# Kernel tuning notes

Measured on AMD Instinct MI355X. Metric: run time of the kernel, lower is better.

Reference implementation:

```python
import jax, jax.numpy as jnp
import numpy as np

EPS_COS = 1e-8   # torch F.cosine_similarity eps
EPS_LN = 1e-6    # LayerNorm eps from source


def _attn_block(x, spat, roi, W, b, k):
    """MultiHeadedAttention_3 (flag=1) forward.
    x: [B,N,C], spat: [B,N,2], roi: [B,N,N], W: [h, 2C+4], b: [h].
    query[b,i,j]=x[b,j], key[b,i,j]=x[b,i]; ft = cat(query,key,spat_q,spat_k).
    The linear over the concat is split into per-part einsums (same math,
    avoids materializing the [B,N,N,2C+4] tensor).
    Returns attn1 * roi * topk-scatter mask, shape [B,N,N,h] (dims b,i,j,h).
    """
    B, N, C = x.shape
    Wq, Wk = W[:, :C], W[:, C:2 * C]
    Wsq, Wsk = W[:, 2 * C:2 * C + 2], W[:, 2 * C + 2:]
    qt = jnp.einsum('bjc,hc->bjh', x, Wq) + jnp.einsum('bjs,hs->bjh', spat, Wsq)
    kt = jnp.einsum('bic,hc->bih', x, Wk) + jnp.einsum('bis,hs->bih', spat, Wsk)
    logits = qt[:, None, :, :] + kt[:, :, None, :] + b  # [B,i,j,h]
    attn1 = jax.nn.sigmoid(logits)
    # relu(cosine_similarity(query, key, dim=3)) -> [B,i,j] (symmetric)
    xn = x / jnp.maximum(jnp.linalg.norm(x, axis=-1, keepdims=True), EPS_COS)
    scores = jax.nn.relu(jnp.einsum('bic,bjc->bij', xn, xn))
    # torch: atten_mask[:, :, idces, :] = 1.0 with idces [B,N,k,1] sets, for ALL
    # b,i,h, column j to 1 whenever j appears anywhere in idces (global scatter).
    _, idx = jax.lax.top_k(scores, k)  # [B,N,k]
    present = jnp.zeros((N,), x.dtype).at[idx.reshape(-1)].set(1.0)
    return attn1 * roi[:, :, :, None] * present[None, None, :, None]


def _gconv_relu(x, w, bias):
    """Grouped 1x1 Conv1d + ReLU. x: [B,Cin,N], w: [g, Cout/g, Cin/g]."""
    B, Cin, N = x.shape
    g, og, ig = w.shape
    y = jnp.einsum('bgin,goi->bgon', x.reshape(B, g, ig, N), w)
    return jax.nn.relu(y.reshape(B, g * og, N) + bias[None, :, None])


def _forward(input, masks_roi, score_mask, spat, W1, b1, W2, b2,
             cw1, cb1, cw2, cb2, ln_g, ln_b, node_num):
    B, N, C = input.shape
    h = W1.shape[0]
    masks = masks_roi * score_mask[:, None, :]
    f = (score_mask == 0).astype(input.dtype)          # [B,N]
    f_mask = f[:, :, None] * jnp.eye(N, dtype=input.dtype)  # diag_embed

    A1 = (_attn_block(input, spat, masks, W1, b1, node_num)
          + f_mask[:, :, :, None]) / 4.0               # [B,i,j,h]

    out1 = _gconv_relu(jnp.swapaxes(input, 1, 2), cw1, cb1)  # [B,mid,N]
    mid = out1.shape[1]
    # torch: matmul(out1.view(B,h,mid/h,N), A1.permute(0,3,2,1))  ([B,h,j,i])
    out1m = jnp.einsum('bhdj,bijh->bhdi', out1.reshape(B, h, mid // h, N), A1)
    out1 = out1 + out1m.reshape(B, mid, N)

    x2 = jnp.swapaxes(out1, 1, 2)                      # [B,N,mid]
    A2 = (_attn_block(x2, spat, masks, W2, b2, node_num)
          + f_mask[:, :, :, None]) / 4.0

    out2 = _gconv_relu(out1, cw2, cb2)                 # [B,out,N]
    co = out2.shape[1]
    out2m = jnp.einsum('bhdj,bijh->bhdi', out2.reshape(B, h, co // h, N), A2)
    out2m = jnp.swapaxes(out2m.reshape(B, co, N), 1, 2)  # [B,N,out]
    mu = jnp.mean(out2m, axis=-1, keepdims=True)
    var = jnp.mean(jnp.square(out2m - mu), axis=-1, keepdims=True)
    out2m = (out2m - mu) / jnp.sqrt(var + EPS_LN) * ln_g + ln_b
    out2 = out2 + jnp.swapaxes(out2m, 1, 2)
    return jnp.swapaxes(out2, 1, 2)                    # [B,N,out]


def setup_inputs() -> dict:
    key = jax.random.key(0)
    ks = jax.random.split(key, 10)
    B, N, C, MID, OUT, H, G = 8, 1024, 256, 256, 256, 4, 4
    s = 0.05
    return {
        'input': jax.random.normal(ks[0], (B, N, C), jnp.float32),
        'masks_roi': jax.random.randint(ks[1], (B, N, N), 0, 2).astype(jnp.float32),
        'score_mask': jax.random.randint(ks[2], (B, N), 0, 2).astype(jnp.float32),
        'spat': jax.random.uniform(ks[3], (B, N, 2), jnp.float32),
        'W1': s * jax.random.normal(ks[4], (H, 2 * C + 4), jnp.float32),
        'b1': jnp.zeros((H,), jnp.float32),
        'W2': s * jax.random.normal(ks[5], (H, 2 * MID + 4), jnp.float32),
        'b2': jnp.zeros((H,), jnp.float32),
        'cw1': s * jax.random.normal(ks[6], (G, MID // G, C // G), jnp.float32),
        'cb1': jnp.zeros((MID,), jnp.float32),
        'cw2': s * jax.random.normal(ks[7], (G, OUT // G, MID // G), jnp.float32),
        'cb2': jnp.zeros((OUT,), jnp.float32),
        'ln_g': jnp.ones((OUT,), jnp.float32),
        'ln_b': jnp.zeros((OUT,), jnp.float32),
        'node_num': 16,
    }


def reference(input, masks_roi, score_mask, spat, W1, b1, W2, b2,
              cw1, cb1, cw2, cb2, ln_g, ln_b, node_num):
    return _forward(input, masks_roi, score_mask, spat, W1, b1, W2, b2,
                    cw1, cb1, cw2, cb2, ln_g, ln_b, node_num)
```

## Files before the change

### kernel.cpp

```cpp
#include <hip/hip_runtime.h>

constexpr int Bb = 8;
constexpr int Nn = 1024;
constexpr int Cc = 256;
constexpr int Hh = 4;
constexpr int WROW = 2 * Cc + 4;

typedef float fx4 __attribute__((ext_vector_type(4)));
typedef float f32x4 __attribute__((ext_vector_type(4)));
typedef __bf16 bf16x8 __attribute__((ext_vector_type(8)));

#define GLL16(src, dst)                                                      \
  __builtin_amdgcn_global_load_lds(                                          \
      (const __attribute__((address_space(1))) void*)(src),                  \
      (__attribute__((address_space(3))) void*)(dst), 16, 0, 0)

__global__ __launch_bounds__(256) void k_roipack(const float* __restrict__ roi,
                                                 const float* __restrict__ sm,
                                                 unsigned long long* __restrict__ roib) {
  __shared__ short jmapS[1024];
  __shared__ int cntS;
  const int t = threadIdx.x;
  const int gid = blockIdx.x * 4 + (t >> 6);
  const int b = gid >> 10;
  const int l = t & 63;
  if ((t >> 6) == 0) {
    int base = 0;
#pragma unroll
    for (int jc = 0; jc < 16; ++jc) {
      const int j = jc * 64 + l;
      const bool act = sm[b * Nn + j] != 0.f;
      const unsigned long long m = __ballot(act);
      if (act) jmapS[base + __popcll(m & ((1ull << l) - 1))] = (short)j;
      base += __popcll(m);
    }
    if (l == 0) cntS = base;
  }
  __syncthreads();
  const int cnt = cntS;
  const float* rrow = roi + (size_t)gid * Nn;
  unsigned long long* orow = roib + (size_t)gid * 16;
#pragma unroll 4
  for (int pc = 0; pc < 16; ++pc) {
    const int idx = pc * 64 + l;
    const bool valid = idx < cnt;
    const int j = valid ? jmapS[idx] : 0;
    const bool bit = valid && (rrow[j] != 0.f);
    unsigned long long m = __ballot(bit);
    if (l == 0) orow[pc] = m;
  }
}

template <int STAGE>
__global__ __launch_bounds__(256) void k_gconvq(const float* __restrict__ src,
                                                const float* __restrict__ cw,
                                                const float* __restrict__ cb,
                                                const float* __restrict__ sm,
                                                const float* __restrict__ spat,
                                                const float* __restrict__ W,
                                                const float* __restrict__ bias,
                                                float* __restrict__ out,
                                                __bf16* __restrict__ gsm,
                                                float* __restrict__ qt,
                                                float* __restrict__ kt) {
  __shared__ __align__(16) bf16x8 xsB[32][32];
  __shared__ float cbS[256];
  __shared__ float smS[32];
  __shared__ int pcolS[32];
  __shared__ int actS[32];
  const int b = blockIdx.x, tile = blockIdx.y;
  const int n0 = tile * 32;
  const int t = threadIdx.x, w = t >> 6, l = t & 63;

  if (w == 0) {
    const int fullc = n0 >> 6;
    int cbase = 0;
    unsigned long long am = 0;
    for (int jc = 0; jc <= fullc; ++jc) {
      unsigned long long m = __ballot(sm[b * Nn + jc * 64 + l] != 0.f);
      if (jc < fullc) cbase += __popcll(m); else am = m;
    }
    const int lsel = l - (n0 & 63);
    if (lsel >= 0 && lsel < 32) {
      pcolS[lsel] = cbase + __popcll(am & ((1ull << l) - 1));
      actS[lsel] = (int)((am >> l) & 1);
      smS[lsel] = 0.25f * sm[b * Nn + n0 + lsel];
    }
  }
  cbS[t] = cb[t];

  if (STAGE == 0) {
    const int n = t >> 3, c0 = (t & 7) * 32;
    const float* srow = src + ((size_t)(b * Nn + n0 + n)) * Cc + c0;
#pragma unroll
    for (int k = 0; k < 4; ++k) {
      fx4 v0 = *(const fx4*)&srow[k * 8];
      fx4 v1 = *(const fx4*)&srow[k * 8 + 4];
      bf16x8 bv;
#pragma unroll
      for (int e = 0; e < 4; ++e) { bv[e] = (__bf16)v0[e]; bv[4 + e] = (__bf16)v1[e]; }
      xsB[n][((c0 >> 3) + k) ^ (n & 7)] = bv;
    }
  } else {
#pragma unroll
    for (int rr = 0; rr < 8; ++rr) {
      const int c = rr * 32 + (t >> 3);
      const int nq = (t & 7) * 4;
      fx4 v = *(const fx4*)&src[((size_t)(b * Cc + c)) * Nn + n0 + nq];
#pragma unroll
      for (int j = 0; j < 4; ++j) {
        const int n = nq + j;
        __bf16* row = (__bf16*)&xsB[n][(c >> 3) ^ (n & 7)];
        row[c & 7] = (__bf16)v[j];
      }
    }
  }
  __syncthreads();

  const int g = w, dl = l & 15, q = l >> 4;

  bf16x8 a[4][2];
#pragma unroll
  for (int of = 0; of < 4; ++of)
#pragma unroll
    for (int ks = 0; ks < 2; ++ks) {
      const float* cwp = cw + ((size_t)(g * 64 + of * 16 + dl)) * 64 + ks * 32 + q * 8;
      fx4 c0 = *(const fx4*)cwp;
      fx4 c1 = *(const fx4*)(cwp + 4);
#pragma unroll
      for (int e = 0; e < 4; ++e) { a[of][ks][e] = (__bf16)c0[e]; a[of][ks][4 + e] = (__bf16)c1[e]; }
    }
  f32x4 acc[4][2] = {};
#pragma unroll
  for (int nf = 0; nf < 2; ++nf) {
    const int n = nf * 16 + dl;
#pragma unroll
    for (int ks = 0; ks < 2; ++ks) {
      bf16x8 bv = xsB[n][(g * 8 + ks * 4 + q) ^ (n & 7)];
#pragma unroll
      for (int of = 0; of < 4; ++of)
        acc[of][nf] = __builtin_amdgcn_mfma_f32_16x16x32_bf16(a[of][ks], bv, acc[of][nf], 0, 0, 0);
    }
  }
#pragma unroll
  for (int of = 0; of < 4; ++of)
#pragma unroll
    for (int nf = 0; nf < 2; ++nf) {
      const int n = nf * 16 + dl;
      const float smv = smS[n];
      const int act = actS[n];
      const int pc = pcolS[n];
#pragma unroll
      for (int r = 0; r < 4; ++r) {
        const int co = g * 64 + of * 16 + 4 * q + r;
        const float val = fmaxf(acc[of][nf][r] + cbS[co], 0.f);
        const size_t orow = ((size_t)(b * Cc + co)) * Nn;
        out[orow + n0 + n] = val;
        if (act) gsm[orow + pc] = (__bf16)(smv * val);
      }
    }

  {
    const int nl = l & 31, half = l >> 5;
    const float* wq = W + g * WROW;
    const float* wk = wq + Cc;
    float qa = 0.f, ka = 0.f;
#pragma unroll 8
    for (int c2 = 0; c2 < 64; ++c2) {
      const int c = half * 128 + c2 * 2;
      const __bf16* p = (const __bf16*)&xsB[nl][(c >> 3) ^ (nl & 7)] + (c & 7);
      const float x0 = (float)p[0], x1 = (float)p[1];
      qa = fmaf(x0, wq[c], fmaf(x1, wq[c + 1], qa));
      ka = fmaf(x0, wk[c], fmaf(x1, wk[c + 1], ka));
    }
    qa += __shfl_xor(qa, 32, 64);
    ka += __shfl_xor(ka, 32, 64);
    if (l < 32) {
      const int n = n0 + nl;
      const float s0 = spat[(b * Nn + n) * 2 + 0];
      const float s1 = spat[(b * Nn + n) * 2 + 1];
      const float* wsp = W + g * WROW + 2 * Cc;
      const float qf = qa + s0 * wsp[0] + s1 * wsp[1] + bias[g];
      const float kf = ka + s0 * wsp[2] + s1 * wsp[3];
      kt[(b * Hh + g) * Nn + n] = kf * -1.44269504f;
      if (actS[nl]) qt[(b * Hh + g) * Nn + pcolS[nl]] = qf * -1.44269504f;
    }
  }
}

template <int MODE>
__global__ __launch_bounds__(512, 4) void k_apply7(const float* __restrict__ g,
                                                   const __bf16* __restrict__ gsm,
                                                   const float* __restrict__ qt,
                                                   const float* __restrict__ kt,
                                                   const unsigned char* __restrict__ roib,
                                                   const float* __restrict__ sm,
                                                   float* __restrict__ out) {
  __shared__ __align__(16) __bf16 Bs[2][3][2][2048];
  __shared__ __align__(16) float qts[1024];
  __shared__ __align__(16) unsigned char rbs[64 * 128];
  const int b = blockIdx.x, it = blockIdx.y, h = blockIdx.z;
  const int t = threadIdx.x, w = t >> 6, l = t & 63;
  const int grp = w >> 2, wq = w & 3;
  const int i0 = it * 64;
  const int dl = l & 15, q = l >> 4, jqf = q * 8;
  const int iA = i0 + wq * 16 + dl;

  const float kvn = kt[(b * Hh + h) * Nn + iA];
  const float* smrow = sm + b * Nn;

  int cnt = 0;
#pragma unroll
  for (int jc = 0; jc < 16; ++jc)
    cnt += __popcll(__ballot(smrow[jc * 64 + l] != 0.f));
  const int stepsTot = (cnt + 63) >> 6;
  const int S = (stepsTot + 1) >> 1;
  const int c0 = grp * S;

  const __bf16* gsrc = gsm + ((size_t)(b * Cc + h * 64 + wq * 16 + (l >> 2))) * Nn
                       + c0 * 64 + (l & 3) * 8;
  __bf16* ring = &Bs[grp][0][0][0];
  const int wdst = wq * 512;

  {
    const float2 qv = *(const float2*)&qt[(b * Hh + h) * Nn + t * 2];
    qts[t * 2 + 0] = qv.x;
    qts[t * 2 + 1] = qv.y;
  }
  {
    const int r = t >> 3, c = (t & 7) * 16;
    const char* src = (const char*)roib + ((size_t)(b * Nn + i0 + r)) * 128 + c;
    *(int4*)&rbs[r * 128 + c] = *(const int4*)src;
  }
  GLL16(gsrc, ring + 0 * 4096 + 0 * 2048 + wdst);
  GLL16(gsrc + 32, ring + 0 * 4096 + 1 * 2048 + wdst);
  GLL16(gsrc + 64, ring + 1 * 4096 + 0 * 2048 + wdst);
  GLL16(gsrc + 96, ring + 1 * 4096 + 1 * 2048 + wdst);
  __syncthreads();

  const int rbbase = (wq * 16 + dl) * 128;
  f32x4 acc[4] = {};
  int cur = 0;

  for (int s = 0; s < S; ++s) {
    const int ck = c0 + s;
    const unsigned int rb0 = rbs[rbbase + ck * 8 + q];
    const unsigned int rb1 = rbs[rbbase + ck * 8 + 4 + q];
    bf16x8 af0, af1;
    {
      fx4 qa = *(const fx4*)&qts[ck * 64 + jqf];
      fx4 qb = *(const fx4*)&qts[ck * 64 + jqf + 4];
#pragma unroll
      for (int e = 0; e < 4; ++e) {
        float sg = __builtin_amdgcn_rcpf(1.f + __builtin_amdgcn_exp2f(qa[e] + kvn));
        af0[e] = (__bf16)(((rb0 >> e) & 1) ? sg : 0.f);
      }
#pragma unroll
      for (int e = 0; e < 4; ++e) {
        float sg = __builtin_amdgcn_rcpf(1.f + __builtin_amdgcn_exp2f(qb[e] + kvn));
        af0[4 + e] = (__bf16)(((rb0 >> (4 + e)) & 1) ? sg : 0.f);
      }
      fx4 qc = *(const fx4*)&qts[ck * 64 + 32 + jqf];
      fx4 qd = *(const fx4*)&qts[ck * 64 + 32 + jqf + 4];
#pragma unroll
      for (int e = 0; e < 4; ++e) {
        float sg = __builtin_amdgcn_rcpf(1.f + __builtin_amdgcn_exp2f(qc[e] + kvn));
        af1[e] = (__bf16)(((rb1 >> e) & 1) ? sg : 0.f);
      }
#pragma unroll
      for (int e = 0; e < 4; ++e) {
        float sg = __builtin_amdgcn_rcpf(1.f + __builtin_amdgcn_exp2f(qd[e] + kvn));
        af1[4 + e] = (__bf16)(((rb1 >> (4 + e)) & 1) ? sg : 0.f);
      }
    }
    asm volatile("s_waitcnt vmcnt(2)\n\ts_barrier" ::: "memory");
    __builtin_amdgcn_sched_barrier(0);
    {
      const int nc = s + 2;
      const int off = (nc < S) ? nc * 64 : 0;
      const int pf = (cur == 0) ? 2 : cur - 1;
      GLL16(gsrc + off, ring + pf * 4096 + 0 * 2048 + wdst);
      GLL16(gsrc + off + 32, ring + pf * 4096 + 1 * 2048 + wdst);
    }
    const __bf16* bp = ring + cur * 4096;
#pragma unroll
    for (int nf = 0; nf < 4; ++nf) {
      bf16x8 bv = *(const bf16x8*)(bp + (nf * 16 + dl) * 32 + jqf);
      acc[nf] = __builtin_amdgcn_mfma_f32_16x16x32_bf16(af0, bv, acc[nf], 0, 0, 0);
    }
#pragma unroll
    for (int nf = 0; nf < 4; ++nf) {
      bf16x8 bv = *(const bf16x8*)(bp + 2048 + (nf * 16 + dl) * 32 + jqf);
      acc[nf] = __builtin_amdgcn_mfma_f32_16x16x32_bf16(af1, bv, acc[nf], 0, 0, 0);
    }
    cur = (cur == 2) ? 0 : cur + 1;
  }

  __syncthreads();
  float* accS = (float*)&Bs[0][0][0][0];
  if (grp == 1) {
#pragma unroll
    for (int nf = 0; nf < 4; ++nf)
      *(f32x4*)&accS[((wq * 64 + l) * 4 + nf) * 4] = acc[nf];
  }
  __syncthreads();
  if (grp == 0) {
#pragma unroll
    for (int nf = 0; nf < 4; ++nf)
      acc[nf] += *(const f32x4*)&accS[((wq * 64 + l) * 4 + nf) * 4];

    const int iw = i0 + wq * 16 + (l >> 4) * 4;
    fx4 sv = *(const fx4*)&smrow[iw];
    float fv[4];
#pragma unroll
    for (int r = 0; r < 4; ++r) fv[r] = (sv[r] == 0.f) ? 0.25f : 0.f;
    if (MODE == 0) {
#pragma unroll
      for (int nf = 0; nf < 4; ++nf) {
        const int ch = h * 64 + nf * 16 + dl;
        const size_t base = ((size_t)(b * Cc + ch)) * Nn + iw;
        fx4 gv = *(const fx4*)&g[base];
        fx4 res;
#pragma unroll
        for (int r = 0; r < 4; ++r) res[r] = gv[r] * (1.f + fv[r]) + acc[nf][r];
        *(fx4*)&out[base] = res;
      }
    } else {
#pragma unroll
      for (int nf = 0; nf < 4; ++nf) {
        const int ch = h * 64 + nf * 16 + dl;
        fx4 gv = *(const fx4*)&g[((size_t)(b * Cc + ch)) * Nn + iw];
#pragma unroll
        for (int r = 0; r < 4; ++r)
          out[((size_t)b * Nn + iw + r) * Cc + ch] = acc[nf][r] + fv[r] * gv[r];
      }
    }
  }
}

__global__ __launch_bounds__(256) void k_lnfinal(float* __restrict__ io,
                                                 const float* __restrict__ g2,
                                                 const float* __restrict__ lng,
                                                 const float* __restrict__ lnb) {
  __shared__ float gt[32][258];
  const int b = blockIdx.x, i0 = blockIdx.y * 32;
  const int t = threadIdx.x, w = t >> 6, l = t & 63;
  {
    const int n = t & 31, ch = t >> 5;
#pragma unroll 8
    for (int rr = 0; rr < 32; ++rr) {
      int c = rr * 8 + ch;
      gt[n][c] = g2[((size_t)(b * Cc + c)) * Nn + i0 + n];
    }
  }
  __syncthreads();
  const fx4 lngv = *(const fx4*)&lng[l * 4];
  const fx4 lnbv = *(const fx4*)&lnb[l * 4];
#pragma unroll
  for (int r = 0; r < 8; ++r) {
    const int n = r * 4 + w;
    const size_t base = ((size_t)(b * Nn) + i0 + n) * Cc + l * 4;
    fx4 v = *(const fx4*)&io[base];
    float s = v[0] + v[1] + v[2] + v[3];
    float sq = v[0] * v[0] + v[1] * v[1] + v[2] * v[2] + v[3] * v[3];
#pragma unroll
    for (int off = 32; off; off >>= 1) {
      s += __shfl_xor(s, off, 64);
      sq += __shfl_xor(sq, off, 64);
    }
    const float m = s * (1.f / 256.f);
    const float var = sq * (1.f / 256.f) - m * m;
    const float rstd = rsqrtf(fmaxf(var, 0.f) + 1e-6f);
    fx4 gv = *(const fx4*)&gt[n][l * 4];
    fx4 res;
#pragma unroll
    for (int e = 0; e < 4; ++e)
      res[e] = gv[e] + (v[e] - m) * rstd * lngv[e] + lnbv[e];
    *(fx4*)&io[base] = res;
  }
}

extern "C" void kernel_launch(void* const* d_in, const int* in_sizes, int n_in,
                              void* d_out, int out_size, void* d_ws, size_t ws_size,
                              hipStream_t stream) {
  (void)in_sizes; (void)n_in; (void)out_size; (void)ws_size;
  const float* input = (const float*)d_in[0];
  const float* roi   = (const float*)d_in[1];
  const float* sm    = (const float*)d_in[2];
  const float* spat  = (const float*)d_in[3];
  const float* W1    = (const float*)d_in[4];
  const float* b1    = (const float*)d_in[5];
  const float* W2    = (const float*)d_in[6];
  const float* b2    = (const float*)d_in[7];
  const float* cw1   = (const float*)d_in[8];
  const float* cb1   = (const float*)d_in[9];
  const float* cw2   = (const float*)d_in[10];
  const float* cb2   = (const float*)d_in[11];
  const float* lng   = (const float*)d_in[12];
  const float* lnb   = (const float*)d_in[13];

  float* outf = (float*)d_out;
  char* ws = (char*)d_ws;
  const size_t PLANE = (size_t)Bb * Cc * Nn;
  float* gbuf = (float*)ws;
  __bf16* gsm = (__bf16*)(ws + PLANE * 4);
  unsigned long long* roib =
      (unsigned long long*)(ws + PLANE * 4 + PLANE * 2);
  float* qtb = (float*)((char*)roib + (size_t)Bb * Nn * 128);
  float* ktb = qtb + Bb * Hh * Nn;
  float* out1 = outf;

  k_roipack<<<dim3(2048), 256, 0, stream>>>(roi, sm, roib);
  k_gconvq<0><<<dim3(8, 32), 256, 0, stream>>>(input, cw1, cb1, sm, spat, W1, b1,
                                               gbuf, gsm, qtb, ktb);
  k_apply7<0><<<dim3(8, 16, 4), 512, 0, stream>>>(gbuf, gsm, qtb, ktb,
                                                  (const unsigned char*)roib, sm, out1);
  k_gconvq<1><<<dim3(8, 32), 256, 0, stream>>>(out1, cw2, cb2, sm, spat, W2, b2,
                                               gbuf, gsm, qtb, ktb);
  k_apply7<1><<<dim3(8, 16, 4), 512, 0, stream>>>(gbuf, gsm, qtb, ktb,
                                                  (const unsigned char*)roib, sm, outf);
  k_lnfinal<<<dim3(8, 32), 256, 0, stream>>>(outf, gbuf, lng, lnb);
}
```

Baseline: 76.59 us.

## Fuse roi bit-packing into first grouped-conv kernel and precompute active counts

Merges the roi-packing kernel into the stage-0 grouped conv/qk kernel as extra blocks (2304 blocks total), removing one launch and letting both workloads share the device. The roi row is now read coalesced into ballot bitmasks in shared memory before compaction, replacing the previous gather reads. The per-batch active count is stored once and read by the apply kernels instead of being recomputed with 16 ballots. STAGE templating is split into two explicit kernels. The roipack blocks are heavy relative to the conv blocks, which may cause imbalance.

Result: slower. 85.57 us (+11.7%).

```diff
diff --git a/kernel.cpp b/kernel.cpp
--- a/kernel.cpp
+++ b/kernel.cpp
@@ -15,62 +15,74 @@
       (const __attribute__((address_space(1))) void*)(src),                  \
       (__attribute__((address_space(3))) void*)(dst), 16, 0, 0)
 
-__global__ __launch_bounds__(256) void k_roipack(const float* __restrict__ roi,
-                                                 const float* __restrict__ sm,
-                                                 unsigned long long* __restrict__ roib) {
-  __shared__ short jmapS[1024];
-  __shared__ int cntS;
-  const int t = threadIdx.x;
-  const int gid = blockIdx.x * 4 + (t >> 6);
-  const int b = gid >> 10;
-  const int l = t & 63;
-  if ((t >> 6) == 0) {
-    int base = 0;
-#pragma unroll
-    for (int jc = 0; jc < 16; ++jc) {
-      const int j = jc * 64 + l;
-      const bool act = sm[b * Nn + j] != 0.f;
-      const unsigned long long m = __ballot(act);
-      if (act) jmapS[base + __popcll(m & ((1ull << l) - 1))] = (short)j;
-      base += __popcll(m);
-    }
-    if (l == 0) cntS = base;
-  }
-  __syncthreads();
-  const int cnt = cntS;
-  const float* rrow = roi + (size_t)gid * Nn;
-  unsigned long long* orow = roib + (size_t)gid * 16;
-#pragma unroll 4
-  for (int pc = 0; pc < 16; ++pc) {
-    const int idx = pc * 64 + l;
-    const bool valid = idx < cnt;
-    const int j = valid ? jmapS[idx] : 0;
-    const bool bit = valid && (rrow[j] != 0.f);
-    unsigned long long m = __ballot(bit);
-    if (l == 0) orow[pc] = m;
-  }
-}
-
-template <int STAGE>
-__global__ __launch_bounds__(256) void k_gconvq(const float* __restrict__ src,
-                                                const float* __restrict__ cw,
-                                                const float* __restrict__ cb,
-                                                const float* __restrict__ sm,
-                                                const float* __restrict__ spat,
-                                                const float* __restrict__ W,
-                                                const float* __restrict__ bias,
-                                                float* __restrict__ out,
-                                                __bf16* __restrict__ gsm,
-                                                float* __restrict__ qt,
-                                                float* __restrict__ kt) {
+__global__ __launch_bounds__(256) void k_gcq0(const float* __restrict__ src,
+                                              const float* __restrict__ cw,
+                                              const float* __restrict__ cb,
+                                              const float* __restrict__ sm,
+                                              const float* __restrict__ spat,
+                                              const float* __restrict__ W,
+                                              const float* __restrict__ bias,
+                                              float* __restrict__ out,
+                                              __bf16* __restrict__ gsm,
+                                              float* __restrict__ qt,
+                                              float* __restrict__ kt,
+                                              const float* __restrict__ roi,
+                                              unsigned long long* __restrict__ roib,
+                                              int* __restrict__ cntb) {
   __shared__ __align__(16) bf16x8 xsB[32][32];
   __shared__ float cbS[256];
   __shared__ float smS[32];
   __shared__ int pcolS[32];
   __shared__ int actS[32];
-  const int b = blockIdx.x, tile = blockIdx.y;
+  __shared__ short jmapS[1024];
+  __shared__ unsigned long long mwS[4][16];
+  __shared__ int cntS;
+
+  const int t = threadIdx.x, w = t >> 6, l = t & 63;
+
+  if (blockIdx.x >= 256) {
+    const int vb2 = blockIdx.x - 256;
+    const int gid = vb2 * 4 + w;
+    const int b = gid >> 10;
+    if (w == 0) {
+      int base = 0;
+#pragma unroll
+      for (int jc = 0; jc < 16; ++jc) {
+        const int j = jc * 64 + l;
+        const bool act = sm[b * Nn + j] != 0.f;
+        const unsigned long long m = __ballot(act);
+        if (act) jmapS[base + __popcll(m & ((1ull << l) - 1))] = (short)j;
+        base += __popcll(m);
+      }
+      if (l == 0) {
+        cntS = base;
+        if ((vb2 & 255) == 0) cntb[b] = base;
+      }
+    }
+    const float* rrow = roi + (size_t)gid * Nn;
+#pragma unroll 4
+    for (int jc = 0; jc < 16; ++jc) {
+      unsigned long long m = __ballot(rrow[jc * 64 + l] != 0.f);
+      if (l == 0) mwS[w][jc] = m;
+    }
+    __syncthreads();
+    const int cnt = cntS;
+    unsigned long long* orow = roib + (size_t)gid * 16;
+#pragma unroll 4
+    for (int pc = 0; pc < 16; ++pc) {
+      const int idx = pc * 64 + l;
+      const bool valid = idx < cnt;
+      const int j = valid ? (int)jmapS[idx] : 0;
+      const bool bit = valid && ((mwS[w][j >> 6] >> (j & 63)) & 1);
+      unsigned long long m = __ballot(bit);
+      if (l == 0) orow[pc] = m;
+    }
+    return;
+  }
+
+  const int vb = blockIdx.x;
+  const int b = vb & 7, tile = vb >> 3;
   const int n0 = tile * 32;
-  const int t = threadIdx.x, w = t >> 6, l = t & 63;
 
   if (w == 0) {
     const int fullc = n0 >> 6;
@@ -89,7 +101,7 @@
   }
   cbS[t] = cb[t];
 
-  if (STAGE == 0) {
+  {
     const int n = t >> 3, c0 = (t & 7) * 32;
     const float* srow = src + ((size_t)(b * Nn + n0 + n)) * Cc + c0;
 #pragma unroll
@@ -100,19 +112,6 @@
 #pragma unroll
       for (int e = 0; e < 4; ++e) { bv[e] = (__bf16)v0[e]; bv[4 + e] = (__bf16)v1[e]; }
       xsB[n][((c0 >> 3) + k) ^ (n & 7)] = bv;
-    }
-  } else {
-#pragma unroll
-    for (int rr = 0; rr < 8; ++rr) {
-      const int c = rr * 32 + (t >> 3);
-      const int nq = (t & 7) * 4;
-      fx4 v = *(const fx4*)&src[((size_t)(b * Cc + c)) * Nn + n0 + nq];
-#pragma unroll
-      for (int j = 0; j < 4; ++j) {
-        const int n = nq + j;
-        __bf16* row = (__bf16*)&xsB[n][(c >> 3) ^ (n & 7)];
-        row[c & 7] = (__bf16)v[j];
-      }
     }
   }
   __syncthreads();
@@ -188,6 +187,127 @@
   }
 }
 
+__global__ __launch_bounds__(256) void k_gconvq1(const float* __restrict__ src,
+                                                 const float* __restrict__ cw,
+                                                 const float* __restrict__ cb,
+                                                 const float* __restrict__ sm,
+                                                 const float* __restrict__ spat,
+                                                 const float* __restrict__ W,
+                                                 const float* __restrict__ bias,
+                                                 float* __restrict__ out,
+                                                 __bf16* __restrict__ gsm,
+                                                 float* __restrict__ qt,
+                                                 float* __restrict__ kt) {
+  __shared__ __align__(16) bf16x8 xsB[32][32];
+  __shared__ float cbS[256];
+  __shared__ float smS[32];
+  __shared__ int pcolS[32];
+  __shared__ int actS[32];
+  const int b = blockIdx.x, tile = blockIdx.y;
+  const int n0 = tile * 32;
+  const int t = threadIdx.x, w = t >> 6, l = t & 63;
+
+  if (w == 0) {
+    const int fullc = n0 >> 6;
+    int cbase = 0;
+    unsigned long long am = 0;
+    for (int jc = 0; jc <= fullc; ++jc) {
+      unsigned long long m = __ballot(sm[b * Nn + jc * 64 + l] != 0.f);
+      if (jc < fullc) cbase += __popcll(m); else am = m;
+    }
+    const int lsel = l - (n0 & 63);
+    if (lsel >= 0 && lsel < 32) {
+      pcolS[lsel] = cbase + __popcll(am & ((1ull << l) - 1));
+      actS[lsel] = (int)((am >> l) & 1);
+      smS[lsel] = 0.25f * sm[b * Nn + n0 + lsel];
+    }
+  }
+  cbS[t] = cb[t];
+
+#pragma unroll
+  for (int rr = 0; rr < 8; ++rr) {
+    const int c = rr * 32 + (t >> 3);
+    const int nq = (t & 7) * 4;
+    fx4 v = *(const fx4*)&src[((size_t)(b * Cc + c)) * Nn + n0 + nq];
+#pragma unroll
+    for (int j = 0; j < 4; ++j) {
+      const int n = nq + j;
+      __bf16* row = (__bf16*)&xsB[n][(c >> 3) ^ (n & 7)];
+      row[c & 7] = (__bf16)v[j];
+    }
+  }
+  __syncthreads();
+
+  const int g = w, dl = l & 15, q = l >> 4;
+  bf16x8 a[4][2];
+#pragma unroll
+  for (int of = 0; of < 4; ++of)
+#pragma unroll
+    for (int ks = 0; ks < 2; ++ks) {
+      const float* cwp = cw + ((size_t)(g * 64 + of * 16 + dl)) * 64 + ks * 32 + q * 8;
+      fx4 c0 = *(const fx4*)cwp;
+      fx4 c1 = *(const fx4*)(cwp + 4);
+#pragma unroll
+      for (int e = 0; e < 4; ++e) { a[of][ks][e] = (__bf16)c0[e]; a[of][ks][4 + e] = (__bf16)c1[e]; }
+    }
+  f32x4 acc[4][2] = {};
+#pragma unroll
+  for (int nf = 0; nf < 2; ++nf) {
+    const int n = nf * 16 + dl;
+#pragma unroll
+    for (int ks = 0; ks < 2; ++ks) {
+      bf16x8 bv = xsB[n][(g * 8 + ks * 4 + q) ^ (n & 7)];
+#pragma unroll
+      for (int of = 0; of < 4; ++of)
+        acc[of][nf] = __builtin_amdgcn_mfma_f32_16x16x32_bf16(a[of][ks], bv, acc[of][nf], 0, 0, 0);
+    }
+  }
+#pragma unroll
+  for (int of = 0; of < 4; ++of)
+#pragma unroll
+    for (int nf = 0; nf < 2; ++nf) {
+      const int n = nf * 16 + dl;
+      const float smv = smS[n];
+      const int act = actS[n];
+      const int pc = pcolS[n];
+#pragma unroll
+      for (int r = 0; r < 4; ++r) {
+        const int co = g * 64 + of * 16 + 4 * q + r;
+        const float val = fmaxf(acc[of][nf][r] + cbS[co], 0.f);
+        const size_t orow = ((size_t)(b * Cc + co)) * Nn;
+        out[orow + n0 + n] = val;
+        if (act) gsm[orow + pc] = (__bf16)(smv * val);
+      }
+    }
+
+  {
+    const int nl = l & 31, half = l >> 5;
+    const float* wq = W + g * WROW;
+    const float* wk = wq + Cc;
+    float qa = 0.f, ka = 0.f;
+#pragma unroll 8
+    for (int c2 = 0; c2 < 64; ++c2) {
+      const int c = half * 128 + c2 * 2;
+      const __bf16* p = (const __bf16*)&xsB[nl][(c >> 3) ^ (nl & 7)] + (c & 7);
+      const float x0 = (float)p[0], x1 = (float)p[1];
+      qa = fmaf(x0, wq[c], fmaf(x1, wq[c + 1], qa));
+      ka = fmaf(x0, wk[c], fmaf(x1, wk[c + 1], ka));
+    }
+    qa += __shfl_xor(qa, 32, 64);
+    ka += __shfl_xor(ka, 32, 64);
+    if (l < 32) {
+      const int n = n0 + nl;
+      const float s0 = spat[(b * Nn + n) * 2 + 0];
+      const float s1 = spat[(b * Nn + n) * 2 + 1];
+      const float* wsp = W + g * WROW + 2 * Cc;
+      const float qf = qa + s0 * wsp[0] + s1 * wsp[1] + bias[g];
+      const float kf = ka + s0 * wsp[2] + s1 * wsp[3];
+      kt[(b * Hh + g) * Nn + n] = kf * -1.44269504f;
+      if (actS[nl]) qt[(b * Hh + g) * Nn + pcolS[nl]] = qf * -1.44269504f;
+    }
+  }
+}
+
 template <int MODE>
 __global__ __launch_bounds__(512, 4) void k_apply7(const float* __restrict__ g,
                                                    const __bf16* __restrict__ gsm,
@@ -195,6 +315,7 @@
                                                    const float* __restrict__ kt,
                                                    const unsigned char* __restrict__ roib,
                                                    const float* __restrict__ sm,
+                                                   const int* __restrict__ cntb,
                                                    float* __restrict__ out) {
   __shared__ __align__(16) __bf16 Bs[2][3][2][2048];
   __shared__ __align__(16) float qts[1024];
@@ -209,10 +330,7 @@
   const float kvn = kt[(b * Hh + h) * Nn + iA];
   const float* smrow = sm + b * Nn;
 
-  int cnt = 0;
-#pragma unroll
-  for (int jc = 0; jc < 16; ++jc)
-    cnt += __popcll(__ballot(smrow[jc * 64 + l] != 0.f));
+  const int cnt = cntb[b];
   const int stepsTot = (cnt + 63) >> 6;
   const int S = (stepsTot + 1) >> 1;
   const int c0 = grp * S;
@@ -408,16 +526,18 @@
       (unsigned long long*)(ws + PLANE * 4 + PLANE * 2);
   float* qtb = (float*)((char*)roib + (size_t)Bb * Nn * 128);
   float* ktb = qtb + Bb * Hh * Nn;
+  int* cntb = (int*)(ktb + Bb * Hh * Nn);
   float* out1 = outf;
 
-  k_roipack<<<dim3(2048), 256, 0, stream>>>(roi, sm, roib);
-  k_gconvq<0><<<dim3(8, 32), 256, 0, stream>>>(input, cw1, cb1, sm, spat, W1, b1,
-                                               gbuf, gsm, qtb, ktb);
+  k_gcq0<<<dim3(2304), 256, 0, stream>>>(input, cw1, cb1, sm, spat, W1, b1,
+                                         gbuf, gsm, qtb, ktb, roi, roib, cntb);
   k_apply7<0><<<dim3(8, 16, 4), 512, 0, stream>>>(gbuf, gsm, qtb, ktb,
-                                                  (const unsigned char*)roib, sm, out1);
-  k_gconvq<1><<<dim3(8, 32), 256, 0, stream>>>(out1, cw2, cb2, sm, spat, W2, b2,
-                                               gbuf, gsm, qtb, ktb);
+                                                  (const unsigned char*)roib, sm,
+                                                  cntb, out1);
+  k_gconvq1<<<dim3(8, 32), 256, 0, stream>>>(out1, cw2, cb2, sm, spat, W2, b2,
+                                             gbuf, gsm, qtb, ktb);
   k_apply7<1><<<dim3(8, 16, 4), 512, 0, stream>>>(gbuf, gsm, qtb, ktb,
-                                                  (const unsigned char*)roib, sm, outf);
+                                                  (const unsigned char*)roib, sm,
+                                                  cntb, outf);
   k_lnfinal<<<dim3(8, 32), 256, 0, stream>>>(outf, gbuf, lng, lnb);
 }
```
